# Performance work log

Hardware: AMD Instinct MI355X
Metric: run time of the kernel (lower is better)

## Reference

```python
import jax, jax.numpy as jnp
import numpy as np
import string

# Schema: relation_in entities = [e1, e1, e0], relation_out entities = [e0, e1]
N0, N1 = 1024, 512          # e0, e1 instance counts
IN_SHAPE = (N1, N1, N0)
OUT_SHAPE = (N0, N1)

# Each partition is a list of blocks (input_dims, output_dims); dims of the
# same block are set equal (diagonal), input-only blocks are pooled (summed),
# output-only blocks are broadcast. Cross-product of per-entity set partitions:
# e0 owns {in2, out0}; e1 owns {in0, in1, out1}.
_E0_PARTS = [
    [((2,), (0,))],
    [((2,), ()), ((), (0,))],
]
_E1_PARTS = [
    [((0,), ()), ((1,), ()), ((), (1,))],
    [((0, 1), ()), ((), (1,))],
    [((0,), (1,)), ((1,), ())],
    [((1,), (1,)), ((0,), ())],
    [((0, 1), (1,))],
]
PARTITIONS = [a + b for a in _E0_PARTS for b in _E1_PARTS]  # 10 params


def _term(X, blocks):
    """Fused diag -> pool -> broadcast -> undiag -> reindex as one einsum + broadcast."""
    letters = string.ascii_letters
    in_sub = [''] * X.ndim
    keep = []  # (letter, representative output position) for blocks with input AND output
    for k, (i, o) in enumerate(blocks):
        c = letters[k]
        for d in i:
            in_sub[d] = c
        if i and o:
            keep.append((c, min(o)))
    keep.sort(key=lambda t: t[1])
    # repeated input letters = diagonal; letters absent from output = pooled sum
    Z = jnp.einsum(''.join(in_sub) + '->' + ''.join(c for c, _ in keep), X)
    shape = [1] * len(OUT_SHAPE)
    for c, rep in keep:
        shape[rep] = OUT_SHAPE[rep]
    Y = jnp.broadcast_to(Z.reshape(shape), OUT_SHAPE)
    # undiag: any block with >1 output position lives on the diagonal
    for i, o in blocks:
        o = sorted(o)
        if len(o) > 1:
            rep = o[0]
            for p in o[1:]:
                n = OUT_SHAPE[p]
                idx_rep = jnp.arange(n).reshape([n if q == rep else 1 for q in range(len(OUT_SHAPE))])
                idx_p = jnp.arange(n).reshape([n if q == p else 1 for q in range(len(OUT_SHAPE))])
                Y = Y * (idx_rep == idx_p).astype(Y.dtype)
    return Y


def setup_inputs() -> dict:
    key = jax.random.key(0)
    k1, k2 = jax.random.split(key)
    X = jax.random.normal(k1, IN_SHAPE, dtype=jnp.float32)
    # stdv = 1/sqrt(in_dim) = 1.0 -> uniform(-1, 1), shape (params, in_dim, out_dim)
    weights = jax.random.uniform(k2, (len(PARTITIONS), 1, 1), dtype=jnp.float32, minval=-1.0, maxval=1.0)
    return {"X": X, "weights": weights}


def reference(X, weights):
    Y = jnp.zeros(OUT_SHAPE, dtype=X.dtype)
    for i, blocks in enumerate(PARTITIONS):
        Y = Y + _term(X, blocks) * weights[i].reshape(-1)
    return Y
```

## Files before the change

kernel.cpp:

```cpp
#include <hip/hip_runtime.h>


#define N0 1024
#define N1 512

#define TBK 32
#define TAK 128
#define NBB 16
#define NAB 4
#define NCB 4

#define OFF_A1  0
#define OFF_A0  (NBB * N1 * N0)
#define OFF_VEC (OFF_A0 + NAB * N1 * N0)
#define OFF_S2  (OFF_VEC)
#define OFF_D   (OFF_VEC + 1024)
#define OFF_R0  (OFF_VEC + 2048)
#define OFF_R1  (OFF_VEC + 2560)
#define OFF_DG  (OFF_VEC + 3072)
#define VEC_FLOATS 3584

__global__ __launch_bounds__(256) void k1_stream(const float* __restrict__ X,
                                                 float* __restrict__ ws) {
    float* A1part = ws + OFF_A1;
    float* A0part = ws + OFF_A0;
    float* S2 = ws + OFF_S2;
    float* R0 = ws + OFF_R0;
    float* R1 = ws + OFF_R1;

    const int id  = blockIdx.x;
    const int tid = threadIdx.x;
    const int cb = id & 3;
    const int bb = (id >> 2) & 15;
    const int ab = id >> 6;
    const int c  = cb * 256 + tid;
    const int b0 = bb * TBK;
    const int a0 = ab * TAK;

    float acc[TBK];
#pragma unroll
    for (int k = 0; k < TBK; k++) acc[k] = 0.f;

    const float* p = X + ((size_t)a0 * N1 + b0) * N0 + c;
    float* a1out = A1part + ((size_t)bb * N1 + a0) * N0 + c;

    for (int ia = 0; ia < TAK; ia++) {
        float v[TBK];
#pragma unroll
        for (int k = 0; k < TBK; k++) v[k] = p[(size_t)k * N0];
        float s = 0.f;
#pragma unroll
        for (int k = 0; k < TBK; k++) { acc[k] += v[k]; s += v[k]; }
        *a1out = s;
#pragma unroll
        for (int off = 32; off > 0; off >>= 1) s += __shfl_xor(s, off);
        if ((tid & 63) == 0) atomicAdd(&R0[a0 + ia], s);
        p += (size_t)N1 * N0;
        a1out += N0;
    }

    float tot = 0.f;
#pragma unroll
    for (int k = 0; k < TBK; k++) tot += acc[k];
    atomicAdd(&S2[c], tot);

#pragma unroll
    for (int k = 0; k < TBK; k++) {
        A0part[((size_t)ab * N1 + (b0 + k)) * N0 + c] = acc[k];
        float w = acc[k];
#pragma unroll
        for (int off = 32; off > 0; off >>= 1) w += __shfl_xor(w, off);
        if ((tid & 63) == 0) atomicAdd(&R1[b0 + k], w);
    }
}

__global__ __launch_bounds__(256) void k3_diag(const float* __restrict__ X,
                                               float* __restrict__ ws) {
    float* D  = ws + OFF_D;
    float* Dg = ws + OFF_DG;
    const int tid = threadIdx.x;
    const int jbase = blockIdx.x * 4;
    float dacc[4] = {0.f, 0.f, 0.f, 0.f};
    __shared__ float red[256];
    for (int r = 0; r < 4; r++) {
        const int j = jbase + r;
        const float* row = X + (size_t)j * (N1 * N0 + N0);
        float pr = 0.f;
#pragma unroll
        for (int q = 0; q < 4; q++) {
            float x = row[tid + 256 * q];
            dacc[q] += x;
            pr += x;
        }
        red[tid] = pr;
        __syncthreads();
        for (int s = 128; s; s >>= 1) {
            if (tid < s) red[tid] += red[tid + s];
            __syncthreads();
        }
        if (tid == 0) Dg[j] = red[0];
        __syncthreads();
    }
#pragma unroll
    for (int q = 0; q < 4; q++) atomicAdd(&D[tid + 256 * q], dacc[q]);
}

__global__ __launch_bounds__(256) void k4_combine(const float* __restrict__ X,
                                                  const float* __restrict__ W,
                                                  const float* __restrict__ ws,
                                                  float* __restrict__ Y) {
    const float* A1part = ws + OFF_A1;
    const float* A0part = ws + OFF_A0;
    const float* S2 = ws + OFF_S2;
    const float* D  = ws + OFF_D;
    const float* R0 = ws + OFF_R0;
    const float* R1 = ws + OFF_R1;
    const float* Dg = ws + OFF_DG;

    const int tid = threadIdx.x;
    const int ct = blockIdx.x & 15;
    const int jt = blockIdx.x >> 4;
    const int c0 = ct * 64, j0 = jt * 64;

    __shared__ float red[256];
    float p0 = 0.f, p1 = 0.f;
    for (int i = tid; i < N0; i += 256) { p0 += S2[i]; p1 += D[i]; }
    red[tid] = p0; __syncthreads();
    for (int s = 128; s; s >>= 1) { if (tid < s) red[tid] += red[tid + s]; __syncthreads(); }
    const float total = red[0]; __syncthreads();
    red[tid] = p1; __syncthreads();
    for (int s = 128; s; s >>= 1) { if (tid < s) red[tid] += red[tid + s]; __syncthreads(); }
    const float diag_total = red[0]; __syncthreads();

    const float w0 = W[0], w1 = W[1], w2 = W[2], w3 = W[3], w4 = W[4];
    const float w5 = W[5], w6 = W[6], w7 = W[7], w8 = W[8], w9 = W[9];

    const int cl = tid & 63;
    const int jr = tid >> 6;
    const int c = c0 + cl;
    const float base_c = w0 * S2[c] + w1 * D[c] + w5 * total + w6 * diag_total;

    __shared__ float T[64][65];
#pragma unroll
    for (int m = 0; m < 16; m++) {
        const int jo = jr * 16 + m;
        const int j = j0 + jo;
        float a1 = 0.f;
#pragma unroll
        for (int t = 0; t < NBB; t++) a1 += A1part[((size_t)t * N1 + j) * N0 + c];
        float a0v = 0.f;
#pragma unroll
        for (int t = 0; t < NAB; t++) a0v += A0part[((size_t)t * N1 + j) * N0 + c];
        const float dgv = X[(size_t)j * (N1 * N0 + N0) + c];
        const float y = base_c + w2 * a1 + w3 * a0v + w4 * dgv
                      + w7 * R0[j] + w8 * R1[j] + w9 * Dg[j];
        T[jo][cl] = y;
    }
    __syncthreads();
#pragma unroll
    for (int m = 0; m < 16; m++) {
        const int crow = jr * 16 + m;
        Y[(size_t)(c0 + crow) * N1 + (j0 + cl)] = T[cl][crow];
    }
}

extern "C" void kernel_launch(void* const* d_in, const int* in_sizes, int n_in,
                              void* d_out, int out_size, void* d_ws, size_t ws_size,
                              hipStream_t stream) {
    const float* X = (const float*)d_in[0];
    const float* W = (const float*)d_in[1];
    float* Y = (float*)d_out;
    float* ws = (float*)d_ws;

    hipMemsetAsync(ws + OFF_VEC, 0, VEC_FLOATS * sizeof(float), stream);

    k1_stream<<<NCB * NBB * NAB, 256, 0, stream>>>(X, ws);
    k3_diag<<<N1 / 4, 256, 0, stream>>>(X, ws);
    k4_combine<<<16 * 8, 256, 0, stream>>>(X, W, ws, Y);
}
```

Before: 1.490 ms.

## Vectorize streaming pass, drop atomics, add separate reduction kernels

The main streaming kernel now loads float4 and splits the a-range across four waves. Per-wave accumulators are combined through shared memory, and the block count doubles to 512. All atomics and the memset are removed. A new kernel reduces the partial A1/A0 buffers into final slabs and row sums, and a misc kernel computes S2, D and the diagonal sums deterministically. The final combine reads single reduced slabs instead of summing 20 partials. The cost is an extra launch, and the serial 512-length loops in the S2/D blocks run on only 8 blocks.

```diff
diff --git a/kernel.cpp b/kernel.cpp
--- a/kernel.cpp
+++ b/kernel.cpp
@@ -5,112 +5,143 @@
 #define N1 512
 
 #define TBK 32
-#define TAK 128
 #define NBB 16
-#define NAB 4
+#define NAB 8
+#define TAK 64
 #define NCB 4
 
-#define OFF_A1  0
-#define OFF_A0  (NBB * N1 * N0)
-#define OFF_VEC (OFF_A0 + NAB * N1 * N0)
-#define OFF_S2  (OFF_VEC)
-#define OFF_D   (OFF_VEC + 1024)
-#define OFF_R0  (OFF_VEC + 2048)
-#define OFF_R1  (OFF_VEC + 2560)
-#define OFF_DG  (OFF_VEC + 3072)
-#define VEC_FLOATS 3584
-
-__global__ __launch_bounds__(256) void k1_stream(const float* __restrict__ X,
-                                                 float* __restrict__ ws) {
-    float* A1part = ws + OFF_A1;
-    float* A0part = ws + OFF_A0;
-    float* S2 = ws + OFF_S2;
-    float* R0 = ws + OFF_R0;
-    float* R1 = ws + OFF_R1;
+#define OFF_A1P 0u
+#define OFF_A0P (16u*512u*1024u)
+#define OFF_A1S (OFF_A0P + 8u*512u*1024u)
+#define OFF_A0S (OFF_A1S + 512u*1024u)
+#define OFF_S2  (OFF_A0S + 512u*1024u)
+#define OFF_D   (OFF_S2 + 1024u)
+#define OFF_R0  (OFF_D + 1024u)
+#define OFF_R1  (OFF_R0 + 512u)
+#define OFF_DG  (OFF_R1 + 512u)
+
+__global__ __launch_bounds__(256, 2) void k1_stream(const float4* __restrict__ Xv,
+                                                    float* __restrict__ ws) {
+    float4* a1p = (float4*)(ws + OFF_A1P);
+    float4* a0p = (float4*)(ws + OFF_A0P);
 
     const int id  = blockIdx.x;
-    const int tid = threadIdx.x;
     const int cb = id & 3;
     const int bb = (id >> 2) & 15;
     const int ab = id >> 6;
-    const int c  = cb * 256 + tid;
+    const int tid = threadIdx.x;
+    const int w = tid >> 6;
+    const int l = tid & 63;
+    const int c4 = cb * 64 + l;
     const int b0 = bb * TBK;
-    const int a0 = ab * TAK;
-
-    float acc[TBK];
-#pragma unroll
-    for (int k = 0; k < TBK; k++) acc[k] = 0.f;
-
-    const float* p = X + ((size_t)a0 * N1 + b0) * N0 + c;
-    float* a1out = A1part + ((size_t)bb * N1 + a0) * N0 + c;
-
-    for (int ia = 0; ia < TAK; ia++) {
-        float v[TBK];
-#pragma unroll
-        for (int k = 0; k < TBK; k++) v[k] = p[(size_t)k * N0];
+
+    float4 acc[TBK];
+#pragma unroll
+    for (int k = 0; k < TBK; k++) acc[k] = make_float4(0.f, 0.f, 0.f, 0.f);
+
+    const int a0w = ab * TAK + w;
+    const float4* p = Xv + ((size_t)(a0w * N1 + b0)) * (N0 / 4) + c4;
+    float4* a1o = a1p + ((size_t)bb * N1 + a0w) * (N0 / 4) + c4;
+
+    for (int i = 0; i < TAK / 4; i++) {
+        float4 s = make_float4(0.f, 0.f, 0.f, 0.f);
+#pragma unroll
+        for (int k = 0; k < TBK; k++) {
+            float4 v = p[(size_t)k * (N0 / 4)];
+            acc[k] += v;
+            s += v;
+        }
+        *a1o = s;
+        p += (size_t)4 * N1 * (N0 / 4);
+        a1o += 4 * (N0 / 4);
+    }
+
+    __shared__ float4 lred[3][4][64];
+    for (int r = 0; r < TBK / 4; r++) {
+        if (w > 0) {
+#pragma unroll
+            for (int q = 0; q < 4; q++) lred[w - 1][q][l] = acc[4 * r + q];
+        }
+        __syncthreads();
+        if (w == 0) {
+#pragma unroll
+            for (int q = 0; q < 4; q++) {
+                float4 t = acc[4 * r + q];
+                t += lred[0][q][l];
+                t += lred[1][q][l];
+                t += lred[2][q][l];
+                a0p[((size_t)ab * N1 + (b0 + 4 * r + q)) * (N0 / 4) + c4] = t;
+            }
+        }
+        __syncthreads();
+    }
+}
+
+__global__ __launch_bounds__(256) void k2_reduce(float* __restrict__ ws) {
+    const int tid = threadIdx.x;
+    __shared__ float red[256];
+    if (blockIdx.x < N1) {
+        const int a = blockIdx.x;
+        const float4* a1p = (const float4*)(ws + OFF_A1P);
+        float4 s = make_float4(0.f, 0.f, 0.f, 0.f);
+#pragma unroll
+        for (int t = 0; t < NBB; t++) s += a1p[((size_t)t * N1 + a) * (N0 / 4) + tid];
+        ((float4*)(ws + OFF_A1S))[(size_t)a * (N0 / 4) + tid] = s;
+        red[tid] = s.x + s.y + s.z + s.w;
+        __syncthreads();
+        for (int st = 128; st; st >>= 1) { if (tid < st) red[tid] += red[tid + st]; __syncthreads(); }
+        if (tid == 0) ws[OFF_R0 + a] = red[0];
+    } else {
+        const int b = blockIdx.x - N1;
+        const float4* a0p = (const float4*)(ws + OFF_A0P);
+        float4 s = make_float4(0.f, 0.f, 0.f, 0.f);
+#pragma unroll
+        for (int t = 0; t < NAB; t++) s += a0p[((size_t)t * N1 + b) * (N0 / 4) + tid];
+        ((float4*)(ws + OFF_A0S))[(size_t)b * (N0 / 4) + tid] = s;
+        red[tid] = s.x + s.y + s.z + s.w;
+        __syncthreads();
+        for (int st = 128; st; st >>= 1) { if (tid < st) red[tid] += red[tid + st]; __syncthreads(); }
+        if (tid == 0) ws[OFF_R1 + b] = red[0];
+    }
+}
+
+__global__ __launch_bounds__(256) void k3_misc(const float* __restrict__ X,
+                                               float* __restrict__ ws) {
+    const int tid = threadIdx.x;
+    const int blk = blockIdx.x;
+    if (blk < 4) {
+        const int c = blk * 256 + tid;
+        const float* a1s = ws + OFF_A1S;
         float s = 0.f;
-#pragma unroll
-        for (int k = 0; k < TBK; k++) { acc[k] += v[k]; s += v[k]; }
-        *a1out = s;
-#pragma unroll
-        for (int off = 32; off > 0; off >>= 1) s += __shfl_xor(s, off);
-        if ((tid & 63) == 0) atomicAdd(&R0[a0 + ia], s);
-        p += (size_t)N1 * N0;
-        a1out += N0;
-    }
-
-    float tot = 0.f;
-#pragma unroll
-    for (int k = 0; k < TBK; k++) tot += acc[k];
-    atomicAdd(&S2[c], tot);
-
-#pragma unroll
-    for (int k = 0; k < TBK; k++) {
-        A0part[((size_t)ab * N1 + (b0 + k)) * N0 + c] = acc[k];
-        float w = acc[k];
-#pragma unroll
-        for (int off = 32; off > 0; off >>= 1) w += __shfl_xor(w, off);
-        if ((tid & 63) == 0) atomicAdd(&R1[b0 + k], w);
-    }
-}
-
-__global__ __launch_bounds__(256) void k3_diag(const float* __restrict__ X,
-                                               float* __restrict__ ws) {
-    float* D  = ws + OFF_D;
-    float* Dg = ws + OFF_DG;
-    const int tid = threadIdx.x;
-    const int jbase = blockIdx.x * 4;
-    float dacc[4] = {0.f, 0.f, 0.f, 0.f};
-    __shared__ float red[256];
-    for (int r = 0; r < 4; r++) {
-        const int j = jbase + r;
-        const float* row = X + (size_t)j * (N1 * N0 + N0);
-        float pr = 0.f;
-#pragma unroll
-        for (int q = 0; q < 4; q++) {
-            float x = row[tid + 256 * q];
-            dacc[q] += x;
-            pr += x;
-        }
-        red[tid] = pr;
-        __syncthreads();
-        for (int s = 128; s; s >>= 1) {
-            if (tid < s) red[tid] += red[tid + s];
+        for (int a = 0; a < N1; a++) s += a1s[(size_t)a * N0 + c];
+        ws[OFF_S2 + c] = s;
+    } else if (blk < 8) {
+        const int c = (blk - 4) * 256 + tid;
+        float s = 0.f;
+        for (int j = 0; j < N1; j++) s += X[(size_t)j * (N1 * N0 + N0) + c];
+        ws[OFF_D + c] = s;
+    } else {
+        const int jb = (blk - 8) * 4;
+        __shared__ float red[256];
+        for (int r = 0; r < 4; r++) {
+            const int j = jb + r;
+            const float* row = X + (size_t)j * (N1 * N0 + N0);
+            float pr = row[tid] + row[tid + 256] + row[tid + 512] + row[tid + 768];
+            red[tid] = pr;
             __syncthreads();
-        }
-        if (tid == 0) Dg[j] = red[0];
-        __syncthreads();
-    }
-#pragma unroll
-    for (int q = 0; q < 4; q++) atomicAdd(&D[tid + 256 * q], dacc[q]);
+            for (int st = 128; st; st >>= 1) { if (tid < st) red[tid] += red[tid + st]; __syncthreads(); }
+            if (tid == 0) ws[OFF_DG + j] = red[0];
+            __syncthreads();
+        }
+    }
 }
 
 __global__ __launch_bounds__(256) void k4_combine(const float* __restrict__ X,
                                                   const float* __restrict__ W,
                                                   const float* __restrict__ ws,
                                                   float* __restrict__ Y) {
-    const float* A1part = ws + OFF_A1;
-    const float* A0part = ws + OFF_A0;
+    const float* A1S = ws + OFF_A1S;
+    const float* A0S = ws + OFF_A0S;
     const float* S2 = ws + OFF_S2;
     const float* D  = ws + OFF_D;
     const float* R0 = ws + OFF_R0;
@@ -145,12 +176,8 @@
     for (int m = 0; m < 16; m++) {
         const int jo = jr * 16 + m;
         const int j = j0 + jo;
-        float a1 = 0.f;
-#pragma unroll
-        for (int t = 0; t < NBB; t++) a1 += A1part[((size_t)t * N1 + j) * N0 + c];
-        float a0v = 0.f;
-#pragma unroll
-        for (int t = 0; t < NAB; t++) a0v += A0part[((size_t)t * N1 + j) * N0 + c];
+        const float a1 = A1S[(size_t)j * N0 + c];
+        const float a0v = A0S[(size_t)j * N0 + c];
         const float dgv = X[(size_t)j * (N1 * N0 + N0) + c];
         const float y = base_c + w2 * a1 + w3 * a0v + w4 * dgv
                       + w7 * R0[j] + w8 * R1[j] + w9 * Dg[j];
@@ -172,9 +199,8 @@
     float* Y = (float*)d_out;
     float* ws = (float*)d_ws;
 
-    hipMemsetAsync(ws + OFF_VEC, 0, VEC_FLOATS * sizeof(float), stream);
-
-    k1_stream<<<NCB * NBB * NAB, 256, 0, stream>>>(X, ws);
-    k3_diag<<<N1 / 4, 256, 0, stream>>>(X, ws);
+    k1_stream<<<NCB * NBB * NAB, 256, 0, stream>>>((const float4*)X, ws);
+    k2_reduce<<<2 * N1, 256, 0, stream>>>(ws);
+    k3_misc<<<8 + N1 / 4, 256, 0, stream>>>(X, ws);
     k4_combine<<<16 * 8, 256, 0, stream>>>(X, W, ws, Y);
 }
```

Result: faster. 1.455 ms (-2.4%).
